# Optimization experiments

Hardware: AMD Instinct MI355X
Metric: run time of the kernel (lower is better)

Reference implementation:

```python
import jax, jax.numpy as jnp
import numpy as np

B, T, H, S = 2, 2048, 16, 64
EMB = H * S  # 1024


def layer_norm(x, g, b, eps=1e-5):
    mu = jnp.mean(x, axis=-1, keepdims=True)
    var = jnp.var(x, axis=-1, keepdims=True)
    return (x - mu) * jax.lax.rsqrt(var + eps) * g + b


def setup_inputs() -> dict:
    key = jax.random.key(0)
    ks = jax.random.split(key, 12)
    sc = 0.02
    return {
        "x": jax.random.normal(ks[0], (B, T, EMB), dtype=jnp.float32),
        "Wkqv": jax.random.normal(ks[1], (S, 3 * S), dtype=jnp.float32) * sc,
        "Wproj": jax.random.normal(ks[2], (EMB, EMB), dtype=jnp.float32) * sc,
        "g1": jnp.ones((EMB,), jnp.float32),
        "b1": jnp.zeros((EMB,), jnp.float32),
        "W1": jax.random.normal(ks[3], (EMB, 4 * EMB), dtype=jnp.float32) * sc,
        "bff1": jnp.zeros((4 * EMB,), jnp.float32),
        "W2": jax.random.normal(ks[4], (4 * EMB, EMB), dtype=jnp.float32) * sc,
        "bff2": jnp.zeros((EMB,), jnp.float32),
        "g2": jnp.ones((EMB,), jnp.float32),
        "b2": jnp.zeros((EMB,), jnp.float32),
    }


def reference(x, Wkqv, Wproj, g1, b1, W1, bff1, W2, bff2, g2, b2):
    Bb, Tt, _ = x.shape
    xh = x.reshape(Bb, Tt, H, S)                     # [B,T,H,S]
    kqv = jnp.einsum('bths,sd->bthd', xh, Wkqv)      # [B,T,H,3S], shared per-head weight
    k, q, v = jnp.split(kqv, 3, axis=-1)             # note order: k, q, v
    scores = jnp.einsum('bihk,bjhk->bijh', q, k) / jnp.sqrt(jnp.float32(S))
    att = jax.nn.softmax(scores, axis=2)             # softmax over key dim j
    res = jnp.einsum('btih,bihs->bths', att, v).reshape(Bb, Tt, EMB)
    mha = res @ Wproj                                # Linear(emb, emb, bias=False)
    x = layer_norm(x + mha, g1, b1)
    h = jax.nn.gelu(x @ W1 + bff1, approximate=False)
    ff = h @ W2 + bff2
    return layer_norm(x + ff, g2, b2)
```

## Files before the change

### kernel.cpp

```cpp
#include <hip/hip_runtime.h>
#include <hip/hip_bf16.h>
#include <math.h>

#define B_ 2
#define T_ 2048
#define H_ 16
#define S_ 64
#define EMB 1024
#define FF 4096
#define BT (B_*T_)
#define ROWS (B_*T_*H_)

typedef __attribute__((ext_vector_type(8))) short s16x8;
typedef __attribute__((ext_vector_type(4))) float f32x4;

struct P4 { unsigned short* p[4]; };

__device__ __forceinline__ unsigned short f2b(float f) {
    return __builtin_bit_cast(unsigned short, __float2bfloat16(f));
}
__device__ __forceinline__ float b2f(short u) {
    return __builtin_bit_cast(float, ((unsigned int)(unsigned short)u) << 16);
}

__device__ __forceinline__ void gl_lds16(const void* g, void* l) {
    __builtin_amdgcn_global_load_lds(
        (const __attribute__((address_space(1))) void*)g,
        (__attribute__((address_space(3))) void*)l, 16, 0, 0);
}

__device__ __forceinline__ f32x4 mfma16(s16x8 a, s16x8 b, f32x4 c) {
    return __builtin_amdgcn_mfma_f32_16x16x32_bf16(a, b, c, 0, 0, 0);
}

#define WAIT_VM8 0x0F78
#define WAIT_VM4 0x0F74
#define WAIT_VM2 0x0F72
#define WAIT_VM0 0x0F70


__global__ __launch_bounds__(256) void kqv_kernel(const float* __restrict__ x,
        const unsigned short* __restrict__ Wqt, unsigned short* __restrict__ K,
        unsigned short* __restrict__ Q, unsigned short* __restrict__ V) {
    const int tid = threadIdx.x;
    const int w = tid >> 6, lane = tid & 63;
    const int l15 = lane & 15, quad = lane >> 4;
    const long r0 = (long)blockIdx.x * 128 + w * 32;

    s16x8 af[2][2];
    #pragma unroll
    for (int mt = 0; mt < 2; ++mt)
        #pragma unroll
        for (int ks = 0; ks < 2; ++ks) {
            const float* xp = x + (r0 + mt*16 + l15) * 64 + ks*32 + quad*8;
            const float4 v0 = *(const float4*)xp;
            const float4 v1 = *(const float4*)(xp + 4);
            s16x8 a;
            a[0] = (short)f2b(v0.x); a[1] = (short)f2b(v0.y);
            a[2] = (short)f2b(v0.z); a[3] = (short)f2b(v0.w);
            a[4] = (short)f2b(v1.x); a[5] = (short)f2b(v1.y);
            a[6] = (short)f2b(v1.z); a[7] = (short)f2b(v1.w);
            af[mt][ks] = a;
        }

    #pragma unroll
    for (int nt = 0; nt < 12; ++nt) {
        const s16x8 b0 = *(const s16x8*)&Wqt[(nt*16 + l15)*64 + quad*8];
        const s16x8 b1 = *(const s16x8*)&Wqt[(nt*16 + l15)*64 + 32 + quad*8];
        f32x4 acc[2] = {};
        #pragma unroll
        for (int mt = 0; mt < 2; ++mt) {
            acc[mt] = mfma16(af[mt][0], b0, acc[mt]);
            acc[mt] = mfma16(af[mt][1], b1, acc[mt]);
        }
        unsigned short* dst = (nt < 4) ? K : (nt < 8) ? Q : V;
        const int c0 = (nt & 3) * 16 + l15;
        #pragma unroll
        for (int mt = 0; mt < 2; ++mt)
            #pragma unroll
            for (int r = 0; r < 4; ++r)
                dst[(r0 + mt*16 + quad*4 + r) * 64 + c0] = f2b(acc[mt][r]);
    }
}

__global__ __launch_bounds__(256) void vt_kernel(const unsigned short* __restrict__ V,
        unsigned short* __restrict__ VT) {
    __shared__ unsigned short Ts[64][72];
    const int tid = threadIdx.x;
    const int tt = blockIdx.x, bh = blockIdx.y;
    const int b = bh >> 4, h = bh & 15;
    const long vbase = ((long)b * (T_*H_) + h) * 64;
    #pragma unroll
    for (int i = 0; i < 2; ++i) {
        const int id = i * 256 + tid;
        const int tr = id >> 3, dc = (id & 7) * 8;
        const s16x8 v = *(const s16x8*)&V[vbase + (long)(tt*64 + tr)*1024 + dc];
        *(s16x8*)&Ts[tr][dc] = v;
    }
    __syncthreads();
    #pragma unroll
    for (int i = 0; i < 2; ++i) {
        const int id = i * 256 + tid;
        const int d = id >> 3, tc = (id & 7) * 8;
        s16x8 o;
        #pragma unroll
        for (int j = 0; j < 8; ++j) o[j] = (short)Ts[tc + j][d];
        *(s16x8*)&VT[((long)bh*64 + d)*2048 + tt*64 + tc] = o;
    }
}

__global__ __launch_bounds__(256) void attn_kernel(const unsigned short* __restrict__ Q,
        const unsigned short* __restrict__ K, const unsigned short* __restrict__ VT,
        unsigned short* __restrict__ Op, float* __restrict__ lp) {
    __shared__ __align__(16) unsigned short Kbuf[2][2][32*32];
    __shared__ __align__(16) unsigned short Vbuf[2][64*32];
    __shared__ __align__(16) unsigned short Ps[4][32*40];
    const int tid = threadIdx.x;
    const int wid = tid >> 6, lane = tid & 63;
    const int l15 = lane & 15, quad = lane >> 4;
    const int bid = blockIdx.x;
    const int s = blockIdx.y;
    const int qg = bid & 15, bh = bid >> 4;
    const long base = ((long)(bh >> 4) * (T_*H_) + (bh & 15)) * 64;
    const unsigned short* Qp = Q + base;
    const unsigned short* Kp = K + base;
    const unsigned short* Vp = VT + (long)bh * 64 * 2048;
    const int q0 = qg * 128 + wid * 32;
    const int kt0 = s * 32;
    unsigned short* ps = &Ps[wid][0];
    const int rk = (l15 >> 1) & 3;
    const int sc8 = ((lane & 3) ^ ((lane >> 3) & 3)) * 8;

    s16x8 qf[2][2];
    #pragma unroll
    for (int qq = 0; qq < 2; ++qq)
        #pragma unroll
        for (int ks = 0; ks < 2; ++ks) {
            const s16x8 raw = *(const s16x8*)&Qp[(long)(q0 + qq*16 + l15)*1024 + ks*32 + quad*8];
            s16x8 q;
            #pragma unroll
            for (int j = 0; j < 8; ++j) q[j] = (short)f2b(b2f(raw[j]) * 0.125f);
            qf[qq][ks] = q;
        }

    s16x8 onef;
    #pragma unroll
    for (int j = 0; j < 8; ++j) onef[j] = (short)0x3F80;

    f32x4 oacc[2][4] = {};
    f32x4 lacc[2] = {};

    const int j16 = lane >> 2;

    auto stage = [&](int bufi, int kt) {
        char* kl = (char*)&Kbuf[bufi][0][0];
        char* vl = (char*)&Vbuf[bufi][0];
        const unsigned short* kg = Kp + (long)(kt*32) * 1024;
        const unsigned short* vg = Vp + kt*32 + sc8;
        switch (wid) {
        case 0:
            gl_lds16(kg + (long)j16*1024 + sc8,           kl +    0 + lane*16);
            gl_lds16(kg + (long)(j16+16)*1024 + sc8,      kl + 1024 + lane*16);
            break;
        case 1:
            gl_lds16(kg + (long)j16*1024 + 32 + sc8,      kl + 2048 + lane*16);
            gl_lds16(kg + (long)(j16+16)*1024 + 32 + sc8, kl + 3072 + lane*16);
            break;
        case 2:
            gl_lds16(vg + (long)(j16     )*2048, vl +    0 + lane*16);
            gl_lds16(vg + (long)(j16 + 16)*2048, vl + 1024 + lane*16);
            break;
        default:
            gl_lds16(vg + (long)(j16 + 32)*2048, vl + 2048 + lane*16);
            gl_lds16(vg + (long)(j16 + 48)*2048, vl + 3072 + lane*16);
            break;
        }
    };

    auto compute = [&](int bufi) {
        f32x4 sT[2][2] = {};
        #pragma unroll
        for (int ks = 0; ks < 2; ++ks)
            #pragma unroll
            for (int jt = 0; jt < 2; ++jt) {
                const s16x8 kf = *(const s16x8*)&Kbuf[bufi][ks][(jt*16 + l15)*32 + (quad ^ rk)*8];
                sT[jt][0] = mfma16(kf, qf[0][ks], sT[jt][0]);
                sT[jt][1] = mfma16(kf, qf[1][ks], sT[jt][1]);
            }
        #pragma unroll
        for (int jt = 0; jt < 2; ++jt)
            #pragma unroll
            for (int qq = 0; qq < 2; ++qq) {
                uint2 pk;
                pk.x = (unsigned int)f2b(__expf(sT[jt][qq][0]))
                     | ((unsigned int)f2b(__expf(sT[jt][qq][1])) << 16);
                pk.y = (unsigned int)f2b(__expf(sT[jt][qq][2]))
                     | ((unsigned int)f2b(__expf(sT[jt][qq][3])) << 16);
                *(uint2*)&ps[(qq*16 + l15)*40 + jt*16 + quad*4] = pk;
            }
        s16x8 pf[2];
        #pragma unroll
        for (int qq = 0; qq < 2; ++qq) {
            pf[qq] = *(const s16x8*)&ps[(qq*16 + l15)*40 + quad*8];
            lacc[qq] = mfma16(pf[qq], onef, lacc[qq]);
        }
        #pragma unroll
        for (int nt = 0; nt < 4; ++nt) {
            const s16x8 vf = *(const s16x8*)&Vbuf[bufi][(nt*16 + l15)*32 + (quad ^ rk)*8];
            oacc[0][nt] = mfma16(pf[0], vf, oacc[0][nt]);
            oacc[1][nt] = mfma16(pf[1], vf, oacc[1][nt]);
        }
    };

    stage(0, kt0);
    for (int kt = 0; kt < 31; ++kt) {
        stage((kt + 1) & 1, kt0 + kt + 1);
        __builtin_amdgcn_s_waitcnt(WAIT_VM2);
        __builtin_amdgcn_s_barrier();
        __builtin_amdgcn_sched_barrier(0);
        compute(kt & 1);
        __builtin_amdgcn_s_barrier();
        __builtin_amdgcn_sched_barrier(0);
    }
    __builtin_amdgcn_s_waitcnt(WAIT_VM0);
    __builtin_amdgcn_s_barrier();
    __builtin_amdgcn_sched_barrier(0);
    compute(1);

    unsigned short* op = Op + ((long)s * 32 + bh) * 2048 * 64;
    float* lrow = lp + ((long)s * 32 + bh) * 2048;
    #pragma unroll
    for (int qq = 0; qq < 2; ++qq)
        #pragma unroll
        for (int r = 0; r < 4; ++r) {
            const int t = q0 + qq*16 + quad*4 + r;
            if (l15 == 0) lrow[t] = lacc[qq][r];
            #pragma unroll
            for (int nt = 0; nt < 4; ++nt)
                op[(long)t*64 + nt*16 + l15] = f2b(oacc[qq][nt][r]);
        }
}

__global__ __launch_bounds__(256) void attn_combine(const unsigned short* __restrict__ Op,
        const float* __restrict__ lp, unsigned short* __restrict__ res) {
    const int gid = blockIdx.x * 256 + threadIdx.x;
    const int row = gid >> 4;
    const int c4 = (gid & 15) * 4;
    const int bh = row >> 11, t = row & 2047;
    const int b = bh >> 4, h = bh & 15;
    const float inv = 1.f / (lp[row] + lp[ROWS + row]);
    const ushort4 u0 = *(const ushort4*)&Op[(long)row * 64 + c4];
    const ushort4 u1 = *(const ushort4*)&Op[((long)ROWS + row) * 64 + c4];
    unsigned short* r = res + ((long)(b*T_ + t)) * EMB + h*64 + c4;
    r[0] = f2b((b2f((short)u0.x) + b2f((short)u1.x)) * inv);
    r[1] = f2b((b2f((short)u0.y) + b2f((short)u1.y)) * inv);
    r[2] = f2b((b2f((short)u0.z) + b2f((short)u1.z)) * inv);
    r[3] = f2b((b2f((short)u0.w) + b2f((short)u1.w)) * inv);
}

__global__ __launch_bounds__(256) void gemm_gelu(const unsigned short* __restrict__ A,
        const unsigned short* __restrict__ Bt, const float* __restrict__ bias,
        unsigned short* __restrict__ C, int M, int N, int Kd) {
    __shared__ __align__(16) unsigned short As[2][128 * 32];
    __shared__ __align__(16) unsigned short Bs[2][128 * 32];
    const int tid = threadIdx.x;
    const int w = tid >> 6, lane = tid & 63;
    const int l15 = lane & 15, quad = lane >> 4;
    const int wm = w >> 1, wn = w & 1;
    const int bn = blockIdx.x, bm = blockIdx.y;
    const int sr = lane >> 2;
    const int sskq = (lane & 3) ^ ((lane >> 3) & 3);
    const int rk = (l15 >> 1) & 3;
    f32x4 acc[4][4] = {};
    const long arow = (long)(bm*128 + w*32 + sr);
    const long brow = (long)(bn*128 + w*32 + sr);

    auto stage = [&](int bi, int kt) {
        char* as = (char*)&As[bi][0];
        char* bs = (char*)&Bs[bi][0];
        gl_lds16(A  + (arow     )*Kd + kt + sskq*8, as + (w*32     )*64 + lane*16);
        gl_lds16(A  + (arow + 16)*Kd + kt + sskq*8, as + (w*32 + 16)*64 + lane*16);
        gl_lds16(Bt + (brow     )*Kd + kt + sskq*8, bs + (w*32     )*64 + lane*16);
        gl_lds16(Bt + (brow + 16)*Kd + kt + sskq*8, bs + (w*32 + 16)*64 + lane*16);
    };

    const int NT = Kd >> 5;
    stage(0, 0);
    int bi = 0;
    for (int t = 0; t < NT; ++t) {
        if (t + 1 < NT) {
            stage(bi ^ 1, (t + 1) * 32);
            __builtin_amdgcn_s_waitcnt(WAIT_VM4);
        } else {
            __builtin_amdgcn_s_waitcnt(WAIT_VM0);
        }
        __builtin_amdgcn_s_barrier();
        __builtin_amdgcn_sched_barrier(0);
        s16x8 af[4], bf[4];
        #pragma unroll
        for (int mt = 0; mt < 4; ++mt)
            af[mt] = *(const s16x8*)&As[bi][(wm*64 + mt*16 + l15)*32 + (quad ^ rk)*8];
        #pragma unroll
        for (int nt = 0; nt < 4; ++nt)
            bf[nt] = *(const s16x8*)&Bs[bi][(wn*64 + nt*16 + l15)*32 + (quad ^ rk)*8];
        #pragma unroll
        for (int mt = 0; mt < 4; ++mt)
            #pragma unroll
            for (int nt = 0; nt < 4; ++nt)
                acc[mt][nt] = mfma16(af[mt], bf[nt], acc[mt][nt]);
        __builtin_amdgcn_s_barrier();
        __builtin_amdgcn_sched_barrier(0);
        bi ^= 1;
    }

    #pragma unroll
    for (int mt = 0; mt < 4; ++mt) {
        const int row0 = bm*128 + wm*64 + mt*16 + quad*4;
        #pragma unroll
        for (int nt = 0; nt < 4; ++nt) {
            const int col = bn*128 + wn*64 + nt*16 + l15;
            const float bv = bias[col];
            #pragma unroll
            for (int r = 0; r < 4; ++r) {
                float v = acc[mt][nt][r] + bv;
                v = 0.5f * v * (1.f + erff(v * 0.70710678118654752440f));
                C[(long)(row0 + r)*N + col] = f2b(v);
            }
        }
    }
}

__global__ __launch_bounds__(256) void gemm_splitk(const unsigned short* __restrict__ A,
        const unsigned short* __restrict__ Bt, P4 parts, int M, int N, int Kd, int Ks) {
    __shared__ __align__(16) unsigned short As[2][128 * 32];
    __shared__ __align__(16) unsigned short Bs[2][128 * 32];
    const int tid = threadIdx.x;
    const int w = tid >> 6, lane = tid & 63;
    const int l15 = lane & 15, quad = lane >> 4;
    const int wm = w >> 1, wn = w & 1;
    const int bn = blockIdx.x, bm = blockIdx.y, s = blockIdx.z;
    const int sr = lane >> 2;
    const int sskq = (lane & 3) ^ ((lane >> 3) & 3);
    const int rk = (l15 >> 1) & 3;
    f32x4 acc[4][4] = {};
    const long arow = (long)(bm*128 + w*32 + sr);
    const long brow = (long)(bn*128 + w*32 + sr);
    const int k0 = s * Ks;

    auto stage = [&](int bi, int kt) {
        char* as = (char*)&As[bi][0];
        char* bs = (char*)&Bs[bi][0];
        gl_lds16(A  + (arow     )*Kd + kt + sskq*8, as + (w*32     )*64 + lane*16);
        gl_lds16(A  + (arow + 16)*Kd + kt + sskq*8, as + (w*32 + 16)*64 + lane*16);
        gl_lds16(Bt + (brow     )*Kd + kt + sskq*8, bs + (w*32     )*64 + lane*16);
        gl_lds16(Bt + (brow + 16)*Kd + kt + sskq*8, bs + (w*32 + 16)*64 + lane*16);
    };

    const int NT = Ks >> 5;
    stage(0, k0);
    int bi = 0;
    for (int t = 0; t < NT; ++t) {
        if (t + 1 < NT) {
            stage(bi ^ 1, k0 + (t + 1) * 32);
            __builtin_amdgcn_s_waitcnt(WAIT_VM4);
        } else {
            __builtin_amdgcn_s_waitcnt(WAIT_VM0);
        }
        __builtin_amdgcn_s_barrier();
        __builtin_amdgcn_sched_barrier(0);
        s16x8 af[4], bf[4];
        #pragma unroll
        for (int mt = 0; mt < 4; ++mt)
            af[mt] = *(const s16x8*)&As[bi][(wm*64 + mt*16 + l15)*32 + (quad ^ rk)*8];
        #pragma unroll
        for (int nt = 0; nt < 4; ++nt)
            bf[nt] = *(const s16x8*)&Bs[bi][(wn*64 + nt*16 + l15)*32 + (quad ^ rk)*8];
        #pragma unroll
        for (int mt = 0; mt < 4; ++mt)
            #pragma unroll
            for (int nt = 0; nt < 4; ++nt)
                acc[mt][nt] = mfma16(af[mt], bf[nt], acc[mt][nt]);
        __builtin_amdgcn_s_barrier();
        __builtin_amdgcn_sched_barrier(0);
        bi ^= 1;
    }

    unsigned short* Cp = parts.p[s];
    #pragma unroll
    for (int mt = 0; mt < 4; ++mt) {
        const int row0 = bm*128 + wm*64 + mt*16 + quad*4;
        #pragma unroll
        for (int nt = 0; nt < 4; ++nt) {
            const int col = bn*128 + wn*64 + nt*16 + l15;
            #pragma unroll
            for (int r = 0; r < 4; ++r)
                Cp[(long)(row0 + r)*N + col] = f2b(acc[mt][nt][r]);
        }
    }
}

template <int P, int XBF>
__global__ __launch_bounds__(256) void ln_kernel(const void* __restrict__ xa,
        P4 parts, const float* __restrict__ addb, const float* __restrict__ g,
        const float* __restrict__ bia, float* __restrict__ out,
        unsigned short* __restrict__ outb) {
    const int row = blockIdx.x;
    const int tid = threadIdx.x;
    float4 v;
    if (XBF) {
        const ushort4 u = ((const ushort4*)xa)[(long)row * (EMB/4) + tid];
        v.x = b2f((short)u.x); v.y = b2f((short)u.y);
        v.z = b2f((short)u.z); v.w = b2f((short)u.w);
    } else {
        v = ((const float4*)xa)[(long)row * (EMB/4) + tid];
    }
    #pragma unroll
    for (int p = 0; p < P; ++p) {
        const ushort4 u = ((const ushort4*)(parts.p[p] + (long)row * EMB))[tid];
        v.x += b2f((short)u.x); v.y += b2f((short)u.y);
        v.z += b2f((short)u.z); v.w += b2f((short)u.w);
    }
    if (addb) {
        const float4 ab = ((const float4*)addb)[tid];
        v.x += ab.x; v.y += ab.y; v.z += ab.z; v.w += ab.w;
    }
    float s = v.x + v.y + v.z + v.w;
    float ss = v.x * v.x + v.y * v.y + v.z * v.z + v.w * v.w;
    #pragma unroll
    for (int off = 32; off > 0; off >>= 1) {
        s += __shfl_down(s, off, 64);
        ss += __shfl_down(ss, off, 64);
    }
    __shared__ float ls[4], lss[4];
    __shared__ float mean_s, rstd_s;
    const int wid = tid >> 6, lane = tid & 63;
    if (lane == 0) { ls[wid] = s; lss[wid] = ss; }
    __syncthreads();
    if (tid == 0) {
        const float S0 = ls[0] + ls[1] + ls[2] + ls[3];
        const float S2 = lss[0] + lss[1] + lss[2] + lss[3];
        const float mean = S0 * (1.f / EMB);
        const float var = S2 * (1.f / EMB) - mean * mean;
        mean_s = mean;
        rstd_s = rsqrtf(var + 1e-5f);
    }
    __syncthreads();
    const float mean = mean_s, rstd = rstd_s;
    const float4 gg = ((const float4*)g)[tid];
    const float4 bb = ((const float4*)bia)[tid];
    float4 o;
    o.x = (v.x - mean) * rstd * gg.x + bb.x;
    o.y = (v.y - mean) * rstd * gg.y + bb.y;
    o.z = (v.z - mean) * rstd * gg.z + bb.z;
    o.w = (v.w - mean) * rstd * gg.w + bb.w;
    if (out) ((float4*)(out + (long)row * EMB))[tid] = o;
    if (outb) {
        unsigned short* ob = outb + (long)row * EMB + tid * 4;
        ob[0] = f2b(o.x); ob[1] = f2b(o.y); ob[2] = f2b(o.z); ob[3] = f2b(o.w);
    }
}

__global__ __launch_bounds__(256) void transp_all(const float* __restrict__ Wp,
        const float* __restrict__ W1, const float* __restrict__ W2,
        const float* __restrict__ Wq, unsigned short* __restrict__ Wpt,
        unsigned short* __restrict__ W1t, unsigned short* __restrict__ W2t,
        unsigned short* __restrict__ Wqt) {
    int id = blockIdx.x;
    const float* W; unsigned short* Wt; int Kd, N, ntx;
    if (id < 1024)      {            W = Wp; Wt = Wpt; Kd = 1024; N = 1024; ntx = 32; }
    else if (id < 5120) { id -= 1024; W = W1; Wt = W1t; Kd = 1024; N = 4096; ntx = 128; }
    else if (id < 9216) { id -= 5120; W = W2; Wt = W2t; Kd = 4096; N = 1024; ntx = 32; }
    else                { id -= 9216; W = Wq; Wt = Wqt; Kd = 64;   N = 192;  ntx = 6;  }
    __shared__ float Ts[32][33];
    const int tid = threadIdx.x;
    const int n0 = (id % ntx) * 32, k0 = (id / ntx) * 32;
    const int r = tid >> 3, c4 = (tid & 7) * 4;
    const float4 v = *(const float4*)&W[(long)(k0 + r) * N + n0 + c4];
    Ts[r][c4] = v.x; Ts[r][c4 + 1] = v.y; Ts[r][c4 + 2] = v.z; Ts[r][c4 + 3] = v.w;
    __syncthreads();
    #pragma unroll
    for (int i = 0; i < 4; ++i)
        Wt[(long)(n0 + r) * Kd + k0 + c4 + i] = f2b(Ts[c4 + i][r]);
}

extern "C" void kernel_launch(void* const* d_in, const int* in_sizes, int n_in,
                              void* d_out, int out_size, void* d_ws, size_t ws_size,
                              hipStream_t stream) {
    (void)in_sizes; (void)n_in; (void)out_size;
    const float* x     = (const float*)d_in[0];
    const float* Wkqv  = (const float*)d_in[1];
    const float* Wproj = (const float*)d_in[2];
    const float* g1    = (const float*)d_in[3];
    const float* b1    = (const float*)d_in[4];
    const float* W1    = (const float*)d_in[5];
    const float* bff1  = (const float*)d_in[6];
    const float* W2    = (const float*)d_in[7];
    const float* bff2  = (const float*)d_in[8];
    const float* g2    = (const float*)d_in[9];
    const float* b2    = (const float*)d_in[10];
    float* out = (float*)d_out;
    char* ws = (char*)d_ws;

    const size_t MB = 1u << 20;
    unsigned short* Qb   = (unsigned short*)(ws + 0 * MB);
    unsigned short* Kb   = (unsigned short*)(ws + 8 * MB);
    unsigned short* Vb   = (unsigned short*)(ws + 16 * MB);
    unsigned short* resb = (unsigned short*)(ws + 24 * MB);
    unsigned short* hb   = (unsigned short*)(ws + 8 * MB);
    unsigned short* VTb  = (unsigned short*)(ws + 40 * MB);
    unsigned short* mp0  = (unsigned short*)(ws + 40 * MB);
    unsigned short* mp1  = (unsigned short*)(ws + 48 * MB);
    unsigned short* Opb  = (unsigned short*)(ws + 48 * MB);
    float*          lpb  = (float*)         (ws + 64 * MB);
    unsigned short* x1b  = Qb;
    unsigned short* Wpt  = (unsigned short*)(ws + 72 * MB);
    unsigned short* W1t  = (unsigned short*)(ws + 74 * MB);
    unsigned short* W2t  = (unsigned short*)(ws + 82 * MB);
    unsigned short* Wqt  = (unsigned short*)(ws + 90 * MB);
    unsigned short* fp2  = (unsigned short*)(ws + 91 * MB);
    unsigned short* fp3  = (unsigned short*)(ws + 99 * MB);
    const bool big = ws_size >= 108 * MB;

    transp_all<<<dim3(9228), 256, 0, stream>>>(Wproj, W1, W2, Wkqv, Wpt, W1t, W2t, Wqt);

    kqv_kernel<<<dim3(ROWS/128), 256, 0, stream>>>(x, Wqt, Kb, Qb, Vb);
    vt_kernel<<<dim3(T_/64, B_*H_), 256, 0, stream>>>(Vb, VTb);
    attn_kernel<<<dim3(512, 2), 256, 0, stream>>>(Qb, Kb, VTb, Opb, lpb);
    attn_combine<<<dim3(ROWS*16/256), 256, 0, stream>>>(Opb, lpb, resb);
    P4 mp; mp.p[0] = mp0; mp.p[1] = mp1; mp.p[2] = nullptr; mp.p[3] = nullptr;
    gemm_splitk<<<dim3(EMB/128, BT/128, 2), 256, 0, stream>>>(resb, Wpt, mp, BT, EMB, EMB, EMB/2);
    ln_kernel<2, 0><<<dim3(BT), 256, 0, stream>>>(x, mp, nullptr, g1, b1, nullptr, x1b);
    gemm_gelu<<<dim3(FF/128, BT/128), 256, 0, stream>>>(x1b, W1t, bff1, hb, BT, FF, EMB);
    if (big) {
        P4 fp; fp.p[0] = mp0; fp.p[1] = mp1; fp.p[2] = fp2; fp.p[3] = fp3;
        gemm_splitk<<<dim3(EMB/128, BT/128, 4), 256, 0, stream>>>(hb, W2t, fp, BT, EMB, FF, FF/4);
        ln_kernel<4, 1><<<dim3(BT), 256, 0, stream>>>(x1b, fp, bff2, g2, b2, out, nullptr);
    } else {
        P4 fp; fp.p[0] = mp0; fp.p[1] = mp1; fp.p[2] = nullptr; fp.p[3] = nullptr;
        gemm_splitk<<<dim3(EMB/128, BT/128, 2), 256, 0, stream>>>(hb, W2t, fp, BT, EMB, FF, FF/2);
        ln_kernel<2, 1><<<dim3(BT), 256, 0, stream>>>(x1b, fp, bff2, g2, b2, out, nullptr);
    }
}
```

Measured before the change: 334.1 us.

## Load GEMM fragments directly from global into registers, dropping LDS staging

Both bf16 GEMM kernels (GELU FFN and split-K) stop staging A/B tiles through double-buffered LDS via global_load_lds and barriers. Each wave now loads its own MFMA fragments straight from global memory into registers, with a two-stage register ping-pong prefetch. This removes LDS traffic and workgroup barriers, but each wave re-reads A rows shared with its sibling wave. The per-lane 16-byte loads are also strided across rows, which relies on L1/L2 to absorb the redundancy and uncoalesced access.

```diff
diff --git a/kernel.cpp b/kernel.cpp
--- a/kernel.cpp
+++ b/kernel.cpp
@@ -33,11 +33,8 @@
     return __builtin_amdgcn_mfma_f32_16x16x32_bf16(a, b, c, 0, 0, 0);
 }
 
-#define WAIT_VM8 0x0F78
-#define WAIT_VM4 0x0F74
 #define WAIT_VM2 0x0F72
 #define WAIT_VM0 0x0F70
-
 
 __global__ __launch_bounds__(256) void kqv_kernel(const float* __restrict__ x,
         const unsigned short* __restrict__ Wqt, unsigned short* __restrict__ K,
@@ -261,56 +258,52 @@
 __global__ __launch_bounds__(256) void gemm_gelu(const unsigned short* __restrict__ A,
         const unsigned short* __restrict__ Bt, const float* __restrict__ bias,
         unsigned short* __restrict__ C, int M, int N, int Kd) {
-    __shared__ __align__(16) unsigned short As[2][128 * 32];
-    __shared__ __align__(16) unsigned short Bs[2][128 * 32];
     const int tid = threadIdx.x;
     const int w = tid >> 6, lane = tid & 63;
     const int l15 = lane & 15, quad = lane >> 4;
     const int wm = w >> 1, wn = w & 1;
     const int bn = blockIdx.x, bm = blockIdx.y;
-    const int sr = lane >> 2;
-    const int sskq = (lane & 3) ^ ((lane >> 3) & 3);
-    const int rk = (l15 >> 1) & 3;
     f32x4 acc[4][4] = {};
-    const long arow = (long)(bm*128 + w*32 + sr);
-    const long brow = (long)(bn*128 + w*32 + sr);
-
-    auto stage = [&](int bi, int kt) {
-        char* as = (char*)&As[bi][0];
-        char* bs = (char*)&Bs[bi][0];
-        gl_lds16(A  + (arow     )*Kd + kt + sskq*8, as + (w*32     )*64 + lane*16);
-        gl_lds16(A  + (arow + 16)*Kd + kt + sskq*8, as + (w*32 + 16)*64 + lane*16);
-        gl_lds16(Bt + (brow     )*Kd + kt + sskq*8, bs + (w*32     )*64 + lane*16);
-        gl_lds16(Bt + (brow + 16)*Kd + kt + sskq*8, bs + (w*32 + 16)*64 + lane*16);
-    };
+
+    const unsigned short* ap[4];
+    const unsigned short* bp[4];
+    #pragma unroll
+    for (int mt = 0; mt < 4; ++mt)
+        ap[mt] = A + (long)(bm*128 + wm*64 + mt*16 + l15)*Kd + quad*8;
+    #pragma unroll
+    for (int nt = 0; nt < 4; ++nt)
+        bp[nt] = Bt + (long)(bn*128 + wn*64 + nt*16 + l15)*Kd + quad*8;
 
     const int NT = Kd >> 5;
-    stage(0, 0);
-    int bi = 0;
-    for (int t = 0; t < NT; ++t) {
-        if (t + 1 < NT) {
-            stage(bi ^ 1, (t + 1) * 32);
-            __builtin_amdgcn_s_waitcnt(WAIT_VM4);
-        } else {
-            __builtin_amdgcn_s_waitcnt(WAIT_VM0);
-        }
-        __builtin_amdgcn_s_barrier();
-        __builtin_amdgcn_sched_barrier(0);
-        s16x8 af[4], bf[4];
+    s16x8 afA[4], bfA[4], afB[4], bfB[4];
+    #pragma unroll
+    for (int i = 0; i < 4; ++i) {
+        afA[i] = *(const s16x8*)(ap[i]);
+        bfA[i] = *(const s16x8*)(bp[i]);
+    }
+    for (int t = 0; t < NT; t += 2) {
+        const int k1 = (t + 1) * 32;
+        #pragma unroll
+        for (int i = 0; i < 4; ++i) {
+            afB[i] = *(const s16x8*)(ap[i] + k1);
+            bfB[i] = *(const s16x8*)(bp[i] + k1);
+        }
         #pragma unroll
         for (int mt = 0; mt < 4; ++mt)
-            af[mt] = *(const s16x8*)&As[bi][(wm*64 + mt*16 + l15)*32 + (quad ^ rk)*8];
-        #pragma unroll
-        for (int nt = 0; nt < 4; ++nt)
-            bf[nt] = *(const s16x8*)&Bs[bi][(wn*64 + nt*16 + l15)*32 + (quad ^ rk)*8];
+            #pragma unroll
+            for (int nt = 0; nt < 4; ++nt)
+                acc[mt][nt] = mfma16(afA[mt], bfA[nt], acc[mt][nt]);
+        const int k2 = (t + 2 < NT) ? (t + 2) * 32 : 0;
+        #pragma unroll
+        for (int i = 0; i < 4; ++i) {
+            afA[i] = *(const s16x8*)(ap[i] + k2);
+            bfA[i] = *(const s16x8*)(bp[i] + k2);
+        }
         #pragma unroll
         for (int mt = 0; mt < 4; ++mt)
             #pragma unroll
             for (int nt = 0; nt < 4; ++nt)
-                acc[mt][nt] = mfma16(af[mt], bf[nt], acc[mt][nt]);
-        __builtin_amdgcn_s_barrier();
-        __builtin_amdgcn_sched_barrier(0);
-        bi ^= 1;
+                acc[mt][nt] = mfma16(afB[mt], bfB[nt], acc[mt][nt]);
     }
 
     #pragma unroll
@@ -332,57 +325,53 @@
 
 __global__ __launch_bounds__(256) void gemm_splitk(const unsigned short* __restrict__ A,
         const unsigned short* __restrict__ Bt, P4 parts, int M, int N, int Kd, int Ks) {
-    __shared__ __align__(16) unsigned short As[2][128 * 32];
-    __shared__ __align__(16) unsigned short Bs[2][128 * 32];
     const int tid = threadIdx.x;
     const int w = tid >> 6, lane = tid & 63;
     const int l15 = lane & 15, quad = lane >> 4;
     const int wm = w >> 1, wn = w & 1;
     const int bn = blockIdx.x, bm = blockIdx.y, s = blockIdx.z;
-    const int sr = lane >> 2;
-    const int sskq = (lane & 3) ^ ((lane >> 3) & 3);
-    const int rk = (l15 >> 1) & 3;
     f32x4 acc[4][4] = {};
-    const long arow = (long)(bm*128 + w*32 + sr);
-    const long brow = (long)(bn*128 + w*32 + sr);
     const int k0 = s * Ks;
 
-    auto stage = [&](int bi, int kt) {
-        char* as = (char*)&As[bi][0];
-        char* bs = (char*)&Bs[bi][0];
-        gl_lds16(A  + (arow     )*Kd + kt + sskq*8, as + (w*32     )*64 + lane*16);
-        gl_lds16(A  + (arow + 16)*Kd + kt + sskq*8, as + (w*32 + 16)*64 + lane*16);
-        gl_lds16(Bt + (brow     )*Kd + kt + sskq*8, bs + (w*32     )*64 + lane*16);
-        gl_lds16(Bt + (brow + 16)*Kd + kt + sskq*8, bs + (w*32 + 16)*64 + lane*16);
-    };
+    const unsigned short* ap[4];
+    const unsigned short* bp[4];
+    #pragma unroll
+    for (int mt = 0; mt < 4; ++mt)
+        ap[mt] = A + (long)(bm*128 + wm*64 + mt*16 + l15)*Kd + k0 + quad*8;
+    #pragma unroll
+    for (int nt = 0; nt < 4; ++nt)
+        bp[nt] = Bt + (long)(bn*128 + wn*64 + nt*16 + l15)*Kd + k0 + quad*8;
 
     const int NT = Ks >> 5;
-    stage(0, k0);
-    int bi = 0;
-    for (int t = 0; t < NT; ++t) {
-        if (t + 1 < NT) {
-            stage(bi ^ 1, k0 + (t + 1) * 32);
-            __builtin_amdgcn_s_waitcnt(WAIT_VM4);
-        } else {
-            __builtin_amdgcn_s_waitcnt(WAIT_VM0);
-        }
-        __builtin_amdgcn_s_barrier();
-        __builtin_amdgcn_sched_barrier(0);
-        s16x8 af[4], bf[4];
+    s16x8 afA[4], bfA[4], afB[4], bfB[4];
+    #pragma unroll
+    for (int i = 0; i < 4; ++i) {
+        afA[i] = *(const s16x8*)(ap[i]);
+        bfA[i] = *(const s16x8*)(bp[i]);
+    }
+    for (int t = 0; t < NT; t += 2) {
+        const int k1 = (t + 1) * 32;
+        #pragma unroll
+        for (int i = 0; i < 4; ++i) {
+            afB[i] = *(const s16x8*)(ap[i] + k1);
+            bfB[i] = *(const s16x8*)(bp[i] + k1);
+        }
         #pragma unroll
         for (int mt = 0; mt < 4; ++mt)
-            af[mt] = *(const s16x8*)&As[bi][(wm*64 + mt*16 + l15)*32 + (quad ^ rk)*8];
-        #pragma unroll
-        for (int nt = 0; nt < 4; ++nt)
-            bf[nt] = *(const s16x8*)&Bs[bi][(wn*64 + nt*16 + l15)*32 + (quad ^ rk)*8];
+            #pragma unroll
+            for (int nt = 0; nt < 4; ++nt)
+                acc[mt][nt] = mfma16(afA[mt], bfA[nt], acc[mt][nt]);
+        const int k2 = (t + 2 < NT) ? (t + 2) * 32 : 0;
+        #pragma unroll
+        for (int i = 0; i < 4; ++i) {
+            afA[i] = *(const s16x8*)(ap[i] + k2);
+            bfA[i] = *(const s16x8*)(bp[i] + k2);
+        }
         #pragma unroll
         for (int mt = 0; mt < 4; ++mt)
             #pragma unroll
             for (int nt = 0; nt < 4; ++nt)
-                acc[mt][nt] = mfma16(af[mt], bf[nt], acc[mt][nt]);
-        __builtin_amdgcn_s_barrier();
-        __builtin_amdgcn_sched_barrier(0);
-        bi ^= 1;
+                acc[mt][nt] = mfma16(afB[mt], bfB[nt], acc[mt][nt]);
     }
 
     unsigned short* Cp = parts.p[s];
```

New measurement: 490.1 us. +46.7%, slower.

## Triple-buffer LDS in GEMM kernels with one barrier per k-step

Applied to the files above, without the earlier changes.

Both the GELU GEMM and the split-K GEMM move from double to triple LDS buffering. Global-to-LDS loads now run two k-tiles ahead and are issued right after the barrier. This drops the second per-iteration barrier and gives loads more time to land before they are consumed. The cost is 1.5x the LDS per block, which can lower the number of resident blocks per CU.

```diff
diff --git a/kernel.cpp b/kernel.cpp
--- a/kernel.cpp
+++ b/kernel.cpp
@@ -33,7 +33,6 @@
     return __builtin_amdgcn_mfma_f32_16x16x32_bf16(a, b, c, 0, 0, 0);
 }
 
-#define WAIT_VM8 0x0F78
 #define WAIT_VM4 0x0F74
 #define WAIT_VM2 0x0F72
 #define WAIT_VM0 0x0F70
@@ -261,8 +260,8 @@
 __global__ __launch_bounds__(256) void gemm_gelu(const unsigned short* __restrict__ A,
         const unsigned short* __restrict__ Bt, const float* __restrict__ bias,
         unsigned short* __restrict__ C, int M, int N, int Kd) {
-    __shared__ __align__(16) unsigned short As[2][128 * 32];
-    __shared__ __align__(16) unsigned short Bs[2][128 * 32];
+    __shared__ __align__(16) unsigned short As[3][128 * 32];
+    __shared__ __align__(16) unsigned short Bs[3][128 * 32];
     const int tid = threadIdx.x;
     const int w = tid >> 6, lane = tid & 63;
     const int l15 = lane & 15, quad = lane >> 4;
@@ -286,31 +285,28 @@
 
     const int NT = Kd >> 5;
     stage(0, 0);
-    int bi = 0;
+    stage(1, 32);
+    int cur = 0;
     for (int t = 0; t < NT; ++t) {
-        if (t + 1 < NT) {
-            stage(bi ^ 1, (t + 1) * 32);
-            __builtin_amdgcn_s_waitcnt(WAIT_VM4);
-        } else {
-            __builtin_amdgcn_s_waitcnt(WAIT_VM0);
-        }
+        if (t + 1 < NT) __builtin_amdgcn_s_waitcnt(WAIT_VM4);
+        else            __builtin_amdgcn_s_waitcnt(WAIT_VM0);
         __builtin_amdgcn_s_barrier();
         __builtin_amdgcn_sched_barrier(0);
+        int nxt = cur + 2; if (nxt >= 3) nxt -= 3;
+        if (t + 2 < NT) stage(nxt, (t + 2) * 32);
         s16x8 af[4], bf[4];
         #pragma unroll
         for (int mt = 0; mt < 4; ++mt)
-            af[mt] = *(const s16x8*)&As[bi][(wm*64 + mt*16 + l15)*32 + (quad ^ rk)*8];
+            af[mt] = *(const s16x8*)&As[cur][(wm*64 + mt*16 + l15)*32 + (quad ^ rk)*8];
         #pragma unroll
         for (int nt = 0; nt < 4; ++nt)
-            bf[nt] = *(const s16x8*)&Bs[bi][(wn*64 + nt*16 + l15)*32 + (quad ^ rk)*8];
+            bf[nt] = *(const s16x8*)&Bs[cur][(wn*64 + nt*16 + l15)*32 + (quad ^ rk)*8];
         #pragma unroll
         for (int mt = 0; mt < 4; ++mt)
             #pragma unroll
             for (int nt = 0; nt < 4; ++nt)
                 acc[mt][nt] = mfma16(af[mt], bf[nt], acc[mt][nt]);
-        __builtin_amdgcn_s_barrier();
-        __builtin_amdgcn_sched_barrier(0);
-        bi ^= 1;
+        cur = cur + 1; if (cur >= 3) cur -= 3;
     }
 
     #pragma unroll
@@ -332,8 +328,8 @@
 
 __global__ __launch_bounds__(256) void gemm_splitk(const unsigned short* __restrict__ A,
         const unsigned short* __restrict__ Bt, P4 parts, int M, int N, int Kd, int Ks) {
-    __shared__ __align__(16) unsigned short As[2][128 * 32];
-    __shared__ __align__(16) unsigned short Bs[2][128 * 32];
+    __shared__ __align__(16) unsigned short As[3][128 * 32];
+    __shared__ __align__(16) unsigned short Bs[3][128 * 32];
     const int tid = threadIdx.x;
     const int w = tid >> 6, lane = tid & 63;
     const int l15 = lane & 15, quad = lane >> 4;
@@ -358,31 +354,28 @@
 
     const int NT = Ks >> 5;
     stage(0, k0);
-    int bi = 0;
+    stage(1, k0 + 32);
+    int cur = 0;
     for (int t = 0; t < NT; ++t) {
-        if (t + 1 < NT) {
-            stage(bi ^ 1, k0 + (t + 1) * 32);
-            __builtin_amdgcn_s_waitcnt(WAIT_VM4);
-        } else {
-            __builtin_amdgcn_s_waitcnt(WAIT_VM0);
-        }
+        if (t + 1 < NT) __builtin_amdgcn_s_waitcnt(WAIT_VM4);
+        else            __builtin_amdgcn_s_waitcnt(WAIT_VM0);
         __builtin_amdgcn_s_barrier();
         __builtin_amdgcn_sched_barrier(0);
+        int nxt = cur + 2; if (nxt >= 3) nxt -= 3;
+        if (t + 2 < NT) stage(nxt, k0 + (t + 2) * 32);
         s16x8 af[4], bf[4];
         #pragma unroll
         for (int mt = 0; mt < 4; ++mt)
-            af[mt] = *(const s16x8*)&As[bi][(wm*64 + mt*16 + l15)*32 + (quad ^ rk)*8];
+            af[mt] = *(const s16x8*)&As[cur][(wm*64 + mt*16 + l15)*32 + (quad ^ rk)*8];
         #pragma unroll
         for (int nt = 0; nt < 4; ++nt)
-            bf[nt] = *(const s16x8*)&Bs[bi][(wn*64 + nt*16 + l15)*32 + (quad ^ rk)*8];
+            bf[nt] = *(const s16x8*)&Bs[cur][(wn*64 + nt*16 + l15)*32 + (quad ^ rk)*8];
         #pragma unroll
         for (int mt = 0; mt < 4; ++mt)
             #pragma unroll
             for (int nt = 0; nt < 4; ++nt)
                 acc[mt][nt] = mfma16(af[mt], bf[nt], acc[mt][nt]);
-        __builtin_amdgcn_s_barrier();
-        __builtin_amdgcn_sched_barrier(0);
-        bi ^= 1;
+        cur = cur + 1; if (cur >= 3) cur -= 3;
     }
 
     unsigned short* Cp = parts.p[s];
```

After: 342.4 us. 2.5% more time.
